# Optimization experiments

Hardware: AMD Instinct MI355X
Metric: run time of the kernel (lower is better)

Reference implementation:

```python
import jax, jax.numpy as jnp
import numpy as np

B, C, D, H = 16, 64, 512, 8
SEQ_LEN, LABEL_LEN, PRED_LEN = 1024, 512, 512
DEC_LEN = LABEL_LEN + PRED_LEN
DFF, KSIZE, FACTOR = 2048, 25, 3
E_LAYERS, D_LAYERS = 2, 1


def _pos_emb(L, d):
    pos = np.arange(L, dtype=np.float32)[:, None]
    div = np.exp(np.arange(0, d, 2, dtype=np.float32) * (-np.log(10000.0) / d))
    pe = np.zeros((L, d), np.float32)
    pe[:, 0::2] = np.sin(pos * div)
    pe[:, 1::2] = np.cos(pos * div)
    return jnp.asarray(pe)


def moving_mean(x, k=KSIZE):
    # AvgPool1d(k, stride=1) with replicate padding of (k-1)//2 at both ends
    pad = (k - 1) // 2
    xp = jnp.concatenate([jnp.repeat(x[:, :1], pad, 1), x, jnp.repeat(x[:, -1:], pad, 1)], axis=1)
    cs = jnp.cumsum(xp, axis=1)
    cs = jnp.concatenate([jnp.zeros_like(cs[:, :1]), cs], axis=1)
    return (cs[:, k:] - cs[:, :-k]) / k


def series_decomp(x):
    mm = moving_mean(x)
    return x - mm, mm


def circ_conv3(x, W):
    # Conv1d kernel=3, circular padding=1, no bias. x [B,L,Cin], W [3,Cin,Cout]
    L = x.shape[1]
    xp = jnp.concatenate([x[:, -1:], x, x[:, :1]], axis=1)
    return sum(jnp.einsum('blc,cd->bld', xp[:, k:k + L], W[k]) for k in range(3))


def my_layernorm(x, g, b):
    # LayerNorm then subtract per-sample mean over the time axis (special seasonal layernorm)
    mu = x.mean(-1, keepdims=True)
    var = x.var(-1, keepdims=True)
    xh = (x - mu) / jnp.sqrt(var + 1e-5) * g + b
    return xh - xh.mean(axis=1, keepdims=True)


def autocorrelation(q, k, v):
    # q,k,v: [B,L,H,E]. FFT cross-correlation, top-k lag selection, time-delay aggregation.
    L = q.shape[1]
    qf = jnp.fft.rfft(q.transpose(0, 2, 3, 1), axis=-1)
    kf = jnp.fft.rfft(k.transpose(0, 2, 3, 1), axis=-1)
    corr = jnp.fft.irfft(qf * jnp.conj(kf), n=L, axis=-1)  # [B,H,E,L]
    top_k = int(FACTOR * np.log(L))
    w, delay = jax.lax.top_k(corr.mean(axis=(1, 2)), top_k)  # [B,K]
    tc = jax.nn.softmax(w, axis=-1)
    vp = v.transpose(0, 2, 3, 1)  # [B,H,E,L]
    base = jnp.arange(L)
    agg = jnp.zeros_like(vp)
    for i in range(top_k):  # small fixed K (= int(factor*log L) = 20)
        idx = (base[None, :] + delay[:, i:i + 1]) % L  # circular shift == gather on doubled values
        pattern = jnp.take_along_axis(vp, idx[:, None, None, :], axis=-1)
        agg = agg + pattern * tc[:, i][:, None, None, None]
    return agg.transpose(0, 3, 1, 2)  # [B,L,H,E]


def ac_layer(q_in, kv_in, Wq, bq, Wk, bk, Wv, bv, Wo, bo):
    Bb, L, _ = q_in.shape
    S = kv_in.shape[1]
    E = D // H
    q = (q_in @ Wq + bq).reshape(Bb, L, H, E)
    k = (kv_in @ Wk + bk).reshape(Bb, S, H, E)
    v = (kv_in @ Wv + bv).reshape(Bb, S, H, E)
    out = autocorrelation(q, k, v)  # L == S by construction here
    return out.reshape(Bb, L, D) @ Wo + bo


def _forward(x_enc, x_dec, enc_emb_w, dec_emb_w, enc_Wq, enc_bq, enc_Wk, enc_bk, enc_Wv, enc_bv, enc_Wo, enc_bo, enc_ff1, enc_ff2, enc_ng, enc_nb, dsa_Wq, dsa_bq, dsa_Wk, dsa_bk, dsa_Wv, dsa_bv, dsa_Wo, dsa_bo, dca_Wq, dca_bq, dca_Wk, dca_bk, dca_Wv, dca_bv, dca_Wo, dca_bo, dec_ff1, dec_ff2, dec_trend_w, proj_w, proj_b):
    mean = jnp.repeat(x_enc.mean(axis=1, keepdims=True), PRED_LEN, axis=1)
    zeros = jnp.zeros((x_dec.shape[0], PRED_LEN, x_dec.shape[2]), x_enc.dtype)
    seasonal_init, trend_init = series_decomp(x_enc)
    trend = jnp.concatenate([trend_init[:, -LABEL_LEN:], mean], axis=1)
    seasonal_init = jnp.concatenate([seasonal_init[:, -LABEL_LEN:], zeros], axis=1)
    # encoder (DataEmbedding_wo_temp = token circular conv + sinusoidal pos, dropout=0)
    x = circ_conv3(x_enc, enc_emb_w) + _pos_emb(SEQ_LEN, D)[None]
    for l in range(E_LAYERS):
        x = x + ac_layer(x, x, enc_Wq[l], enc_bq[l], enc_Wk[l], enc_bk[l], enc_Wv[l], enc_bv[l], enc_Wo[l], enc_bo[l])
        x, _ = series_decomp(x)
        y = jax.nn.gelu(x @ enc_ff1[l], approximate=False) @ enc_ff2[l]
        x, _ = series_decomp(x + y)
    enc_out = my_layernorm(x, enc_ng, enc_nb)
    # decoder
    xd = circ_conv3(seasonal_init, dec_emb_w) + _pos_emb(DEC_LEN, D)[None]
    for l in range(D_LAYERS):
        xd = xd + ac_layer(xd, xd, dsa_Wq[l], dsa_bq[l], dsa_Wk[l], dsa_bk[l], dsa_Wv[l], dsa_bv[l], dsa_Wo[l], dsa_bo[l])
        xd, t1 = series_decomp(xd)
        xd = xd + ac_layer(xd, enc_out, dca_Wq[l], dca_bq[l], dca_Wk[l], dca_bk[l], dca_Wv[l], dca_bv[l], dca_Wo[l], dca_bo[l])
        xd, t2 = series_decomp(xd)
        y = jax.nn.gelu(xd @ dec_ff1[l], approximate=False) @ dec_ff2[l]
        xd, t3 = series_decomp(xd + y)
        trend = trend + circ_conv3(t1 + t2 + t3, dec_trend_w[l])  # trend projection conv
    seasonal = xd @ proj_w + proj_b
    out = trend + seasonal
    return out[:, -PRED_LEN:]


def setup_inputs():
    key = jax.random.key(0)
    ks = iter(jax.random.split(key, 64))
    def n(shape, s=0.02):
        return jax.random.normal(next(ks), shape, jnp.float32) * s
    inp = {}
    inp['x_enc'] = jax.random.normal(next(ks), (B, SEQ_LEN, C), jnp.float32)
    inp['x_dec'] = jax.random.normal(next(ks), (B, DEC_LEN, C), jnp.float32)
    inp['enc_emb_w'] = n((3, C, D))
    inp['dec_emb_w'] = n((3, C, D))
    for p in ['Wq', 'Wk', 'Wv', 'Wo']:
        bp = p.replace('W', 'b')
        inp['enc_' + p] = n((E_LAYERS, D, D)); inp['enc_' + bp] = jnp.zeros((E_LAYERS, D))
        inp['dsa_' + p] = n((D_LAYERS, D, D)); inp['dsa_' + bp] = jnp.zeros((D_LAYERS, D))
        inp['dca_' + p] = n((D_LAYERS, D, D)); inp['dca_' + bp] = jnp.zeros((D_LAYERS, D))
    inp['enc_ff1'] = n((E_LAYERS, D, DFF)); inp['enc_ff2'] = n((E_LAYERS, DFF, D))
    inp['enc_ng'] = jnp.ones((D,), jnp.float32); inp['enc_nb'] = jnp.zeros((D,), jnp.float32)
    inp['dec_ff1'] = n((D_LAYERS, D, DFF)); inp['dec_ff2'] = n((D_LAYERS, DFF, D))
    inp['dec_trend_w'] = n((D_LAYERS, 3, D, C))
    inp['proj_w'] = n((D, C)); inp['proj_b'] = jnp.zeros((C,), jnp.float32)
    return inp


def reference(x_enc, x_dec, enc_emb_w, dec_emb_w, enc_Wq, enc_bq, enc_Wk, enc_bk, enc_Wv, enc_bv, enc_Wo, enc_bo, enc_ff1, enc_ff2, enc_ng, enc_nb, dsa_Wq, dsa_bq, dsa_Wk, dsa_bk, dsa_Wv, dsa_bv, dsa_Wo, dsa_bo, dca_Wq, dca_bq, dca_Wk, dca_bk, dca_Wv, dca_bv, dca_Wo, dca_bo, dec_ff1, dec_ff2, dec_trend_w, proj_w, proj_b):
    return _forward(x_enc, x_dec, enc_emb_w, dec_emb_w, enc_Wq, enc_bq, enc_Wk, enc_bk, enc_Wv, enc_bv, enc_Wo, enc_bo, enc_ff1, enc_ff2, enc_ng, enc_nb, dsa_Wq, dsa_bq, dsa_Wk, dsa_bk, dsa_Wv, dsa_bv, dsa_Wo, dsa_bo, dca_Wq, dca_bq, dca_Wk, dca_bk, dca_Wv, dca_bv, dca_Wo, dca_bo, dec_ff1, dec_ff2, dec_trend_w, proj_w, proj_b)
```

## Files before the change

### kernel.cpp

```cpp
#include <hip/hip_runtime.h>
#include <math.h>

#define B_   16
#define L_   1024
#define C_   64
#define D_   512
#define DFF_ 2048
#define TOPK_ 20

typedef float f4 __attribute__((ext_vector_type(4)));
typedef float f32x4 __attribute__((ext_vector_type(4)));
typedef short bf16x8 __attribute__((ext_vector_type(8)));
typedef unsigned short u16x8 __attribute__((ext_vector_type(8)));

__device__ __forceinline__ unsigned short f2bf(float f) {
    union { float f; unsigned u; } a; a.f = f;
    unsigned r = a.u + 0x7fff + ((a.u >> 16) & 1);
    return (unsigned short)(r >> 16);
}
__device__ __forceinline__ float bf2f(unsigned short h) {
    union { unsigned u; float f; } a; a.u = ((unsigned)h) << 16;
    return a.f;
}

__device__ __forceinline__ void gld16(const void* g, void* l) {
    __builtin_amdgcn_global_load_lds(
        (const __attribute__((address_space(1))) unsigned int*)g,
        (__attribute__((address_space(3))) unsigned int*)l, 16, 0, 0);
}


__global__ __launch_bounds__(256)
void gemm_bf16(const unsigned short* __restrict__ A, const unsigned short* __restrict__ Bt,
               float* __restrict__ Cf, unsigned short* __restrict__ Cb,
               unsigned short* __restrict__ Cl,
               const float* __restrict__ bias, int M, int N, int K, int flags, int nx)
{
    __shared__ unsigned short As[128 * 32];
    __shared__ unsigned short Bs[128 * 32];
    const int tid = threadIdx.x;
    const int wave = tid >> 6, lane = tid & 63;

    int total = gridDim.x;
    int h = blockIdx.x;
    int lidx = h;
    if ((total & 7) == 0) {
        int q = total >> 3;
        lidx = (h & 7) * q + (h >> 3);
    }
    const int bm = (lidx / nx) * 128, bn = (lidx % nx) * 128;
    const int wm = (wave >> 1) << 6, wn = (wave & 1) << 6;

    const int r0 = (wave << 5) + (lane >> 2);
    const int kq = (((lane & 3) ^ ((lane >> 3) & 3)) << 3);
    const unsigned short* Ap0 = A + (size_t)(bm + r0) * K + kq;
    const unsigned short* Ap1 = Ap0 + (size_t)16 * K;
    const unsigned short* Bp0 = Bt + (size_t)(bn + r0) * K + kq;
    const unsigned short* Bp1 = Bp0 + (size_t)16 * K;
    unsigned short* Al0 = &As[(wave << 5) * 32];
    unsigned short* Al1 = &As[((wave << 5) + 16) * 32];
    unsigned short* Bl0 = &Bs[(wave << 5) * 32];
    unsigned short* Bl1 = &Bs[((wave << 5) + 16) * 32];

    const int la = lane & 15, h4 = lane >> 4;
    const int sw = (la >> 1) & 3;
    f32x4 acc[4][4] = {};

    for (int k0 = 0; k0 < K; k0 += 32) {
        gld16(Ap0 + k0, Al0);
        gld16(Ap1 + k0, Al1);
        gld16(Bp0 + k0, Bl0);
        gld16(Bp1 + k0, Bl1);
        __syncthreads();
        bf16x8 a[4], b[4];
#pragma unroll
        for (int i = 0; i < 4; ++i) {
            a[i] = *(const bf16x8*)&As[(wm + i * 16 + la) * 32 + ((h4 ^ sw) << 3)];
            b[i] = *(const bf16x8*)&Bs[(wn + i * 16 + la) * 32 + ((h4 ^ sw) << 3)];
        }
#pragma unroll
        for (int mi = 0; mi < 4; ++mi)
#pragma unroll
            for (int ni = 0; ni < 4; ++ni)
                acc[mi][ni] = __builtin_amdgcn_mfma_f32_16x16x32_bf16(a[mi], b[ni], acc[mi][ni], 0, 0, 0);
        __syncthreads();
    }

#pragma unroll
    for (int mi = 0; mi < 4; ++mi) {
#pragma unroll
        for (int r = 0; r < 4; ++r) {
            int m = bm + wm + mi * 16 + h4 * 4 + r;
#pragma unroll
            for (int ni = 0; ni < 4; ++ni) {
                int n = bn + wn + ni * 16 + la;
                float c = acc[mi][ni][r];
                if (bias) c += bias[n];
                if (flags & 2) c = 0.5f * c * (1.0f + erff(c * 0.70710678118654752f));
                size_t o = (size_t)m * N + n;
                if (Cf) { if (flags & 1) Cf[o] += c; else Cf[o] = c; }
                if (Cb) {
                    unsigned short hb = f2bf(c);
                    Cb[o] = hb;
                    if (Cl) Cl[o] = f2bf(c - bf2f(hb));
                }
            }
        }
    }
}

__global__ __launch_bounds__(256)
void gemm_split(const unsigned short* __restrict__ A, const unsigned short* __restrict__ Bt,
                unsigned short* __restrict__ o0h, unsigned short* __restrict__ o0l, const float* __restrict__ b0,
                unsigned short* __restrict__ o1h, unsigned short* __restrict__ o1l, const float* __restrict__ b1,
                unsigned short* __restrict__ o2h, unsigned short* __restrict__ o2l, const float* __restrict__ b2,
                float* __restrict__ Gz, int M, int N, int K, int nx)
{
    __shared__ unsigned short As[128 * 32];
    __shared__ unsigned short Bs[128 * 32];
    const int tid = threadIdx.x;
    const int wave = tid >> 6, lane = tid & 63;

    int total = gridDim.x;
    int h = blockIdx.x;
    if (Gz && h < 64) Gz[h * 256 + tid] = 0.f;
    int lidx = h;
    if ((total & 7) == 0) {
        int q = total >> 3;
        lidx = (h & 7) * q + (h >> 3);
    }
    const int bm = (lidx / nx) * 128, bn = (lidx % nx) * 128;
    const int wm = (wave >> 1) << 6, wn = (wave & 1) << 6;

    const int sel = bn >> 9;
    unsigned short* oh = sel == 0 ? o0h : (sel == 1 ? o1h : o2h);
    unsigned short* ol = sel == 0 ? o0l : (sel == 1 ? o1l : o2l);
    const float* bias  = sel == 0 ? b0  : (sel == 1 ? b1  : b2);
    const int nb = bn & 511;

    const int r0 = (wave << 5) + (lane >> 2);
    const int kq = (((lane & 3) ^ ((lane >> 3) & 3)) << 3);
    const unsigned short* Ap0 = A + (size_t)(bm + r0) * K + kq;
    const unsigned short* Ap1 = Ap0 + (size_t)16 * K;
    const unsigned short* Bp0 = Bt + (size_t)(bn + r0) * K + kq;
    const unsigned short* Bp1 = Bp0 + (size_t)16 * K;
    unsigned short* Al0 = &As[(wave << 5) * 32];
    unsigned short* Al1 = &As[((wave << 5) + 16) * 32];
    unsigned short* Bl0 = &Bs[(wave << 5) * 32];
    unsigned short* Bl1 = &Bs[((wave << 5) + 16) * 32];

    const int la = lane & 15, h4 = lane >> 4;
    const int sw = (la >> 1) & 3;
    f32x4 acc[4][4] = {};

    for (int k0 = 0; k0 < K; k0 += 32) {
        gld16(Ap0 + k0, Al0);
        gld16(Ap1 + k0, Al1);
        gld16(Bp0 + k0, Bl0);
        gld16(Bp1 + k0, Bl1);
        __syncthreads();
        bf16x8 a[4], b[4];
#pragma unroll
        for (int i = 0; i < 4; ++i) {
            a[i] = *(const bf16x8*)&As[(wm + i * 16 + la) * 32 + ((h4 ^ sw) << 3)];
            b[i] = *(const bf16x8*)&Bs[(wn + i * 16 + la) * 32 + ((h4 ^ sw) << 3)];
        }
#pragma unroll
        for (int mi = 0; mi < 4; ++mi)
#pragma unroll
            for (int ni = 0; ni < 4; ++ni)
                acc[mi][ni] = __builtin_amdgcn_mfma_f32_16x16x32_bf16(a[mi], b[ni], acc[mi][ni], 0, 0, 0);
        __syncthreads();
    }

#pragma unroll
    for (int mi = 0; mi < 4; ++mi) {
#pragma unroll
        for (int r = 0; r < 4; ++r) {
            int m = bm + wm + mi * 16 + h4 * 4 + r;
#pragma unroll
            for (int ni = 0; ni < 4; ++ni) {
                int n2 = nb + wn + ni * 16 + la;
                float c = acc[mi][ni][r] + bias[n2];
                size_t o = (size_t)m * 512 + n2;
                unsigned short hb = f2bf(c);
                oh[o] = hb;
                if (ol) ol[o] = f2bf(c - bf2f(hb));
            }
        }
    }
}

__global__ __launch_bounds__(256)
void tcast_kernel(const float* __restrict__ W, unsigned short* __restrict__ Wt, int R, int Cc)
{
    __shared__ float t[32][33];
    int bx = blockIdx.x * 32, by = blockIdx.y * 32;
    int tx = threadIdx.x & 31, ty = threadIdx.x >> 5;
#pragma unroll
    for (int i = 0; i < 32; i += 8)
        t[ty + i][tx] = W[(size_t)(by + ty + i) * Cc + bx + tx];
    __syncthreads();
#pragma unroll
    for (int i = 0; i < 32; i += 8)
        Wt[(size_t)(bx + ty + i) * R + by + tx] = f2bf(t[tx][ty + i]);
}

struct P16 { const float* p[16]; };
__global__ __launch_bounds__(256)
void tcast_all(P16 srcs, unsigned short* __restrict__ dst)
{
    __shared__ float t[32][33];
    const float* W = srcs.p[blockIdx.z];
    unsigned short* Wt = dst + (size_t)blockIdx.z * 262144;
    int bx = blockIdx.x * 32, by = blockIdx.y * 32;
    int tx = threadIdx.x & 31, ty = threadIdx.x >> 5;
#pragma unroll
    for (int i = 0; i < 32; i += 8)
        t[ty + i][tx] = W[(size_t)(by + ty + i) * 512 + bx + tx];
    __syncthreads();
#pragma unroll
    for (int i = 0; i < 32; i += 8)
        Wt[(size_t)(bx + ty + i) * 512 + by + tx] = f2bf(t[tx][ty + i]);
}

__global__ __launch_bounds__(256)
void emb_kernel(const float* __restrict__ A, const float* __restrict__ W,
                float* __restrict__ Xo, unsigned short* __restrict__ Xb)
{
    __shared__ float As[66][68];
    __shared__ float Ws[3][64][64];
    const int tid = threadIdx.x;
    const int bn = blockIdx.x * 64, bm = blockIdx.y * 64;
    const int base = bm & ~1023;
    for (int i = tid; i < 66 * 64; i += 256) {
        int r = i >> 6, c = i & 63;
        int l = (bm - base) + r - 1;
        if (l < 0) l += 1024; else if (l >= 1024) l -= 1024;
        As[r][c] = A[(size_t)(base + l) * 64 + c];
    }
    for (int i = tid; i < 3 * 64 * 64; i += 256) {
        int tap = i >> 12, rem = i & 4095, k = rem >> 6, c = rem & 63;
        Ws[tap][k][c] = W[((size_t)tap * 64 + k) * 512 + bn + c];
    }
    __syncthreads();
    const int tx = tid & 15, ty = tid >> 4;
    float acc[4][4] = {};
    for (int tap = 0; tap < 3; ++tap)
        for (int k = 0; k < 64; ++k) {
            f4 bv = *(const f4*)&Ws[tap][k][tx * 4];
#pragma unroll
            for (int i = 0; i < 4; ++i) {
                float a = As[ty * 4 + i + tap][k];
#pragma unroll
                for (int j = 0; j < 4; ++j)
                    acc[i][j] = fmaf(a, bv[j], acc[i][j]);
            }
        }
#pragma unroll
    for (int i = 0; i < 4; ++i) {
        int m = bm + ty * 4 + i;
        int l = m & 1023;
#pragma unroll
        for (int j = 0; j < 4; ++j) {
            int n = bn + tx * 4 + j;
            float c = acc[i][j];
            int i2 = n & ~1;
            float div = expf(-(float)i2 * 0.017988946039015984f);
            float ang = (float)l * div;
            c += (n & 1) ? cosf(ang) : sinf(ang);
            size_t o = (size_t)m * 512 + n;
            Xo[o] = c;
            Xb[o] = f2bf(c);
        }
    }
}

__global__ __launch_bounds__(256)
void tail_kernel(const float* __restrict__ TSUM, const float* __restrict__ T1,
                 const float* __restrict__ Wt, const float* __restrict__ pw,
                 float* __restrict__ PC, float* __restrict__ PP)
{
    __shared__ float Ts[18][17];
    __shared__ float T1s[16][17];
    __shared__ float Ws[3][16][64];
    __shared__ float Ps[16][64];
    const int tid = threadIdx.x;
    const int bo = blockIdx.x * 16;
    const int kc = blockIdx.y;
    const int b = bo >> 9;
    const int lbase = (bo & 511) + 512;
    const size_t rowbase = (size_t)b << 10;
    const int tc4 = (tid & 15) * 4;
    const int tr = tid >> 4;
    const int kbeg = kc * 64, kend = kbeg + 64;
    float cacc[4] = {}, pacc[4] = {};

    for (int k0 = kbeg; k0 < kend; k0 += 16) {
        for (int i = tid; i < 18 * 16; i += 256) {
            int r = i >> 4, c = i & 15;
            int l = lbase + r - 1; if (l >= 1024) l -= 1024;
            Ts[r][c] = TSUM[(rowbase + l) * 512 + k0 + c];
        }
        {
            int r = tid >> 4, c = tid & 15;
            T1s[r][c] = T1[(rowbase + lbase + r) * 512 + k0 + c];
        }
        for (int i = tid; i < 3 * 16 * 16; i += 256) {
            int tap = i / 256, rem = i & 255, k = rem >> 4, c4 = (rem & 15) * 4;
            *(f4*)&Ws[tap][k][c4] = *(const f4*)&Wt[((size_t)tap * 512 + k0 + k) * 64 + c4];
        }
        if (tid < 256) {
            int k = tid >> 4, c4 = (tid & 15) * 4;
            *(f4*)&Ps[k][c4] = *(const f4*)&pw[(size_t)(k0 + k) * 64 + c4];
        }
        __syncthreads();
        for (int tap = 0; tap < 3; ++tap)
#pragma unroll
            for (int k = 0; k < 16; ++k) {
                f4 bv = *(const f4*)&Ws[tap][k][tc4];
                float a = Ts[tr + tap][k];
#pragma unroll
                for (int j = 0; j < 4; ++j)
                    cacc[j] = fmaf(a, bv[j], cacc[j]);
            }
#pragma unroll
        for (int k = 0; k < 16; ++k) {
            f4 bv = *(const f4*)&Ps[k][tc4];
            float a = T1s[tr][k];
#pragma unroll
            for (int j = 0; j < 4; ++j)
                pacc[j] = fmaf(a, bv[j], pacc[j]);
        }
        __syncthreads();
    }
    size_t o = ((size_t)kc * 8192 + (bo + tr)) * 64 + tc4;
    *(f4*)&PC[o] = *(f4*)cacc;
    *(f4*)&PP[o] = *(f4*)pacc;
}

__global__ __launch_bounds__(256)
void tailred_kernel(const float* __restrict__ PC, const float* __restrict__ PP,
                    const float* __restrict__ MEANC, const float* __restrict__ pb,
                    float* __restrict__ OUT)
{
    int idx = blockIdx.x * blockDim.x + threadIdx.x;
    int n = idx & 63;
    int b = idx >> 15;
    const size_t S = (size_t)8192 * 64;
    float cs = PC[idx];
    float ps = PP[idx];
#pragma unroll
    for (int s = 1; s < 8; ++s) {
        cs += PC[s * S + idx];
        ps += PP[s * S + idx];
    }
    OUT[idx] = (MEANC[(b << 6) + n] + cs) + (ps + pb[n]);
}

__global__ __launch_bounds__(256)
void corr_mfma(const unsigned short* __restrict__ Qh, const unsigned short* __restrict__ Ql,
               const unsigned short* __restrict__ Kh, const unsigned short* __restrict__ Kl,
               float* __restrict__ G)
{
    __shared__ unsigned short Qhs[128 * 32], Qls[128 * 32], Khs[128 * 32], Kls[128 * 32];
    __shared__ float diagw[4][256];
    const int tid = threadIdx.x;
    const int wave = tid >> 6, lane = tid & 63;

    const int i_ = blockIdx.x;
    const int x_ = i_ & 7, j_ = i_ >> 3;
    const int b = x_ + ((j_ >> 6) << 3);
    const int tile = j_ & 63;
    const int bt = (tile >> 3) * 128, bs = (tile & 7) * 128;

    const int wm = (wave >> 1) << 6, wn = (wave & 1) << 6;
    const size_t boff = (size_t)b << 19;

    const int r0 = (wave << 5) + (lane >> 2);
    const int kq = (((lane & 3) ^ ((lane >> 3) & 3)) << 3);
    const size_t g0 = boff + (size_t)(bt + r0) * 512 + kq;
    const size_t g1 = g0 + (size_t)16 * 512;
    const size_t p0 = boff + (size_t)(bs + r0) * 512 + kq;
    const size_t p1 = p0 + (size_t)16 * 512;
    unsigned short* qh0 = &Qhs[(wave << 5) * 32]; unsigned short* qh1 = &Qhs[((wave << 5) + 16) * 32];
    unsigned short* ql0 = &Qls[(wave << 5) * 32]; unsigned short* ql1 = &Qls[((wave << 5) + 16) * 32];
    unsigned short* kh0 = &Khs[(wave << 5) * 32]; unsigned short* kh1 = &Khs[((wave << 5) + 16) * 32];
    unsigned short* kl0 = &Kls[(wave << 5) * 32]; unsigned short* kl1 = &Kls[((wave << 5) + 16) * 32];

    float* dz = &diagw[0][0];
    dz[tid] = 0.f; dz[tid + 256] = 0.f; dz[tid + 512] = 0.f; dz[tid + 768] = 0.f;

    const int la = lane & 15, h4 = lane >> 4;
    const int sw = (la >> 1) & 3;
    f32x4 acc[4][4] = {};

    for (int k0 = 0; k0 < 512; k0 += 32) {
        gld16(Qh + g0 + k0, qh0); gld16(Qh + g1 + k0, qh1);
        gld16(Ql + g0 + k0, ql0); gld16(Ql + g1 + k0, ql1);
        gld16(Kh + p0 + k0, kh0); gld16(Kh + p1 + k0, kh1);
        gld16(Kl + p0 + k0, kl0); gld16(Kl + p1 + k0, kl1);
        __syncthreads();
        bf16x8 ah[4], al[4], bh[4], bl[4];
#pragma unroll
        for (int i = 0; i < 4; ++i) {
            int ro = (wm + i * 16 + la) * 32 + ((h4 ^ sw) << 3);
            int co = (wn + i * 16 + la) * 32 + ((h4 ^ sw) << 3);
            ah[i] = *(const bf16x8*)&Qhs[ro];
            al[i] = *(const bf16x8*)&Qls[ro];
            bh[i] = *(const bf16x8*)&Khs[co];
            bl[i] = *(const bf16x8*)&Kls[co];
        }
#pragma unroll
        for (int mi = 0; mi < 4; ++mi)
#pragma unroll
            for (int ni = 0; ni < 4; ++ni) {
                acc[mi][ni] = __builtin_amdgcn_mfma_f32_16x16x32_bf16(ah[mi], bh[ni], acc[mi][ni], 0, 0, 0);
                acc[mi][ni] = __builtin_amdgcn_mfma_f32_16x16x32_bf16(ah[mi], bl[ni], acc[mi][ni], 0, 0, 0);
                acc[mi][ni] = __builtin_amdgcn_mfma_f32_16x16x32_bf16(al[mi], bh[ni], acc[mi][ni], 0, 0, 0);
            }
        __syncthreads();
    }

    float rbin[7][4] = {};
#pragma unroll
    for (int mi = 0; mi < 4; ++mi)
#pragma unroll
        for (int ni = 0; ni < 4; ++ni)
#pragma unroll
            for (int r = 0; r < 4; ++r)
                rbin[mi - ni + 3][r] += acc[mi][ni][r];

    const int base = (wm - wn) + 4 * h4 - la + 127;
#pragma unroll
    for (int d = 0; d < 7; ++d)
#pragma unroll
        for (int r = 0; r < 4; ++r)
            atomicAdd(&diagw[wave][base + 16 * (d - 3) + r], rbin[d][r]);
    __syncthreads();
    if (tid < 255) {
        float s = diagw[0][tid] + diagw[1][tid] + diagw[2][tid] + diagw[3][tid];
        int n = (bt - bs + tid - 127) & 1023;
        atomicAdd(&G[(b << 10) + n], s);
    }
}

__global__ __launch_bounds__(256)
void topk_kernel(const float* __restrict__ G, int* __restrict__ delay,
                 float* __restrict__ tc)
{
    __shared__ float vals[1024];
    __shared__ float pw[4];
    __shared__ int   pwi[4];
    __shared__ float wsel[TOPK_];
    __shared__ int   isel[TOPK_];
    const int b = blockIdx.x, tid = threadIdx.x;
    const int lane = tid & 63, wid = tid >> 6;
    for (int i = tid; i < 1024; i += 256) vals[i] = G[(b << 10) + i] * (1.0f / 512.0f);
    __syncthreads();
    for (int it = 0; it < TOPK_; ++it) {
        float bv = -INFINITY; int bi = 0;
#pragma unroll
        for (int u = 0; u < 4; ++u) {
            int i = tid * 4 + u;
            float v = vals[i];
            if (v > bv) { bv = v; bi = i; }
        }
#pragma unroll
        for (int o = 32; o > 0; o >>= 1) {
            float ov = __shfl_xor(bv, o, 64);
            int   oi = __shfl_xor(bi, o, 64);
            if (ov > bv || (ov == bv && oi < bi)) { bv = ov; bi = oi; }
        }
        if (lane == 0) { pw[wid] = bv; pwi[wid] = bi; }
        __syncthreads();
        if (tid == 0) {
            float m = pw[0]; int mi = pwi[0];
#pragma unroll
            for (int t = 1; t < 4; ++t)
                if (pw[t] > m || (pw[t] == m && pwi[t] < mi)) { m = pw[t]; mi = pwi[t]; }
            wsel[it] = m; isel[it] = mi;
            vals[mi] = -INFINITY;
        }
        __syncthreads();
    }
    if (tid == 0) {
        float m = wsel[0];
#pragma unroll
        for (int i = 1; i < TOPK_; ++i) m = fmaxf(m, wsel[i]);
        float e[TOPK_], s = 0.f;
#pragma unroll
        for (int i = 0; i < TOPK_; ++i) { e[i] = expf(wsel[i] - m); s += e[i]; }
        float inv = 1.0f / s;
#pragma unroll
        for (int i = 0; i < TOPK_; ++i) {
            tc[b * TOPK_ + i] = e[i] * inv;
            delay[b * TOPK_ + i] = isel[i];
        }
    }
}

__global__ void agg_kernel(const unsigned short* __restrict__ V, const int* __restrict__ delay,
                           const float* __restrict__ tc, unsigned short* __restrict__ out)
{
    int idx = (blockIdx.x * blockDim.x + threadIdx.x) * 8;
    int d = idx & 511;
    int l = (idx >> 9) & 1023;
    int b = idx >> 19;
    const unsigned short* Vb = V + ((size_t)b << 19);
    float s[8] = {};
#pragma unroll
    for (int i = 0; i < TOPK_; ++i) {
        int row = (l + delay[b * TOPK_ + i]) & 1023;
        float w = tc[b * TOPK_ + i];
        u16x8 v = *(const u16x8*)&Vb[((size_t)row << 9) + d];
#pragma unroll
        for (int j = 0; j < 8; ++j)
            s[j] = fmaf(w, bf2f(v[j]), s[j]);
    }
    u16x8 o;
#pragma unroll
    for (int j = 0; j < 8; ++j) o[j] = f2bf(s[j]);
    *(u16x8*)&out[idx] = o;
}

__global__ void decomp_kernel(const float* __restrict__ x, float* __restrict__ seas,
                              unsigned short* __restrict__ seasb,
                              float* __restrict__ trend, int Bn, int Ln, int Ch,
                              int nseg, int tmode)
{
    int idx = blockIdx.x * blockDim.x + threadIdx.x;
    int total = Bn * Ch * nseg;
    if (idx >= total) return;
    int ch = idx % Ch;
    int rest = idx / Ch;
    int seg = rest % nseg;
    int b = rest / nseg;
    int segL = Ln / nseg;
    int l0 = seg * segL;
    const float* xp = x + (size_t)b * Ln * Ch + ch;
    float* sp = seas + (size_t)b * Ln * Ch + ch;
    unsigned short* bp = seasb ? seasb + (size_t)b * Ln * Ch + ch : nullptr;
    float* tp = trend ? trend + (size_t)b * Ln * Ch + ch : nullptr;
    float s = 0.f;
    for (int j = -12; j <= 12; ++j) {
        int t = l0 + j;
        t = t < 0 ? 0 : (t > Ln - 1 ? Ln - 1 : t);
        s += xp[(size_t)t * Ch];
    }
    for (int l = l0; l < l0 + segL; ++l) {
        float mm = s * (1.0f / 25.0f);
        float v = xp[(size_t)l * Ch] - mm;
        sp[(size_t)l * Ch] = v;
        if (bp) bp[(size_t)l * Ch] = f2bf(v);
        if (tmode == 1) tp[(size_t)l * Ch] = mm;
        else if (tmode == 2) tp[(size_t)l * Ch] += mm;
        int ta = l + 13; if (ta > Ln - 1) ta = Ln - 1;
        int ts = l - 12; if (ts < 0) ts = 0;
        s += xp[(size_t)ta * Ch] - xp[(size_t)ts * Ch];
    }
}

__global__ __launch_bounds__(256)
void lnrow_kernel(const float* __restrict__ x, const float* __restrict__ g,
                  const float* __restrict__ bv, float* __restrict__ out)
{
    __shared__ float sh1[4], sh2[4];
    int row = blockIdx.x, tid = threadIdx.x;
    const float* xr = x + ((size_t)row << 9);
    float v0 = xr[tid], v1 = xr[tid + 256];
    float s = v0 + v1, q = v0 * v0 + v1 * v1;
#pragma unroll
    for (int o = 32; o > 0; o >>= 1) {
        s += __shfl_down(s, o, 64);
        q += __shfl_down(q, o, 64);
    }
    int wid = tid >> 6;
    if ((tid & 63) == 0) { sh1[wid] = s; sh2[wid] = q; }
    __syncthreads();
    if (tid == 0) {
        sh1[0] = sh1[0] + sh1[1] + sh1[2] + sh1[3];
        sh2[0] = sh2[0] + sh2[1] + sh2[2] + sh2[3];
    }
    __syncthreads();
    float mu = sh1[0] * (1.0f / 512.0f);
    float var = sh2[0] * (1.0f / 512.0f) - mu * mu;
    float inv = rsqrtf(var + 1e-5f);
    out[((size_t)row << 9) + tid] = (v0 - mu) * inv * g[tid] + bv[tid];
    out[((size_t)row << 9) + tid + 256] = (v1 - mu) * inv * g[tid + 256] + bv[tid + 256];
}

__global__ void colmean_kernel(const float* __restrict__ x, float* __restrict__ m)
{
    int idx = blockIdx.x * blockDim.x + threadIdx.x;
    if (idx >= B_ * D_) return;
    int b = idx >> 9, d = idx & 511;
    const float* xp = x + ((size_t)b << 19) + d;
    float s = 0.f;
    for (int l = 0; l < L_; ++l) s += xp[(size_t)l << 9];
    m[idx] = s * (1.0f / 1024.0f);
}

__global__ void colsub_kernel(const float* __restrict__ x, const float* __restrict__ m,
                              unsigned short* __restrict__ out)
{
    int idx = blockIdx.x * blockDim.x + threadIdx.x;
    int d = idx & 511;
    int b = idx >> 19;
    out[idx] = f2bf(x[idx] - m[(b << 9) + d]);
}

__global__ void meanx_kernel(const float* __restrict__ x, float* __restrict__ m)
{
    int idx = blockIdx.x * blockDim.x + threadIdx.x;
    if (idx >= B_ * C_) return;
    int b = idx >> 6, c = idx & 63;
    const float* xp = x + (size_t)b * L_ * C_ + c;
    float s = 0.f;
    for (int l = 0; l < L_; ++l) s += xp[(size_t)l << 6];
    m[idx] = s * (1.0f / 1024.0f);
}

__global__ void builddec_kernel(const float* __restrict__ seenc, float* __restrict__ seasin)
{
    int idx = blockIdx.x * blockDim.x + threadIdx.x;
    int c = idx & 63;
    int l = (idx >> 6) & 1023;
    int b = idx >> 16;
    if (l < 512) {
        int src = (b << 16) + ((512 + l) << 6) + c;
        seasin[idx] = seenc[src];
    } else {
        seasin[idx] = 0.f;
    }
}

extern "C" void kernel_launch(void* const* d_in, const int* in_sizes, int n_in,
                              void* d_out, int out_size, void* d_ws, size_t ws_size,
                              hipStream_t stream)
{
    auto F = [&](int i) { return (const float*)d_in[i]; };
    const float* x_enc     = F(0);
    const float* enc_emb_w = F(2);
    const float* dec_emb_w = F(3);
    const float* enc_Wq = F(4);  const float* enc_bq = F(5);
    const float* dsa_Wq = F(6);  const float* dsa_bq = F(7);
    const float* dca_Wq = F(8);  const float* dca_bq = F(9);
    const float* enc_Wk = F(10); const float* enc_bk = F(11);
    const float* dsa_Wk = F(12); const float* dsa_bk = F(13);
    const float* dca_Wk = F(14); const float* dca_bk = F(15);
    const float* enc_Wv = F(16); const float* enc_bv = F(17);
    const float* dsa_Wv = F(18); const float* dsa_bv = F(19);
    const float* dca_Wv = F(20); const float* dca_bv = F(21);
    const float* enc_Wo = F(22); const float* enc_bo = F(23);
    const float* dsa_Wo = F(24); const float* dsa_bo = F(25);
    const float* dca_Wo = F(26); const float* dca_bo = F(27);
    const float* enc_ff1 = F(28); const float* enc_ff2 = F(29);
    const float* enc_ng = F(30);  const float* enc_nb = F(31);
    const float* dec_ff1 = F(32); const float* dec_ff2 = F(33);
    const float* dec_trend_w = F(34);
    const float* proj_w = F(35);  const float* proj_b = F(36);

    constexpr size_t F512 = (size_t)B_ * L_ * D_;
    constexpr size_t F64  = (size_t)B_ * L_ * C_;
    constexpr size_t SMALL = 1024 + 16384 + 320 + 320 + 8192;
    constexpr size_t WTSA_N = 16 * 262144;
    constexpr size_t WTSF_N = 2 * 1024 * 1024;
    size_t need = (3 * F512 + 2 * F64 + SMALL) * 4 + (8 * F512 + WTSA_N + WTSF_N) * 2;
    if (ws_size < need) return;

    float* X      = (float*)d_ws;
    float* T1     = X + F512;
    float* TSUM   = T1 + F512;
    float* SEASIN = TSUM + F512;
    float* TREND  = SEASIN + F64;
    float* MEANC  = TREND + F64;
    float* G      = MEANC + 1024;
    float* TCW    = G + 16384;
    int*   DEL    = (int*)(TCW + 320);
    float* LNMEAN = (float*)(DEL + 320);
    unsigned short* AB   = (unsigned short*)(LNMEAN + 8192);
    unsigned short* EB   = AB + F512;
    unsigned short* VB   = EB + F512;
    unsigned short* HB   = VB + F512;
    unsigned short* QHI  = HB + F512;
    unsigned short* QLO  = QHI + F512;
    unsigned short* KHI  = QLO + F512;
    unsigned short* KLO  = KHI + F512;
    unsigned short* WTSA = KLO + F512;
    unsigned short* WTSF = WTSA + WTSA_N;
    float* OUT = (float*)d_out;

    const int M = B_ * L_;

    auto mgemm = [&](const unsigned short* A, const unsigned short* Bt, float* Cf,
                     unsigned short* Cb, unsigned short* Cl, const float* bias,
                     int Mm, int Nn, int Kk, int flags) {
        int nx = Nn / 128;
        int total = nx * (Mm / 128);
        gemm_bf16<<<total, 256, 0, stream>>>(A, Bt, Cf, Cb, Cl, bias, Mm, Nn, Kk, flags, nx);
    };
    auto tcast = [&](const float* W, unsigned short* Wt, int R, int Cc) {
        tcast_kernel<<<dim3(Cc / 32, R / 32), 256, 0, stream>>>(W, Wt, R, Cc);
    };
    auto corr_topk_agg = [&]() {
        corr_mfma<<<1024, 256, 0, stream>>>(QHI, QLO, KHI, KLO, G);
        topk_kernel<<<16, 256, 0, stream>>>(G, DEL, TCW);
        agg_kernel<<<(int)(F512 / 8 / 256), 256, 0, stream>>>(VB, DEL, TCW, HB);
    };
    auto attn_self = [&](const unsigned short* xin, int slotbase,
                         const float* bq, const float* bk, const float* bvp, const float* bo,
                         float* resid) {
        gemm_split<<<12 * 128, 256, 0, stream>>>(xin, WTSA + (size_t)slotbase * 262144,
            QHI, QLO, bq, KHI, KLO, bk, VB, nullptr, bvp, G, M, 1536, 512, 12);
        corr_topk_agg();
        mgemm(HB, WTSA + (size_t)(slotbase + 3) * 262144, resid, nullptr, nullptr, bo, M, 512, 512, 1);
    };
    auto attn_cross = [&](const unsigned short* qin, const unsigned short* kvin, int slotbase,
                          const float* bq, const float* bk, const float* bvp, const float* bo,
                          float* resid) {
        mgemm(qin, WTSA + (size_t)slotbase * 262144, nullptr, QHI, QLO, bq, M, 512, 512, 0);
        gemm_split<<<8 * 128, 256, 0, stream>>>(kvin, WTSA + (size_t)(slotbase + 1) * 262144,
            KHI, KLO, bk, VB, nullptr, bvp, nullptr, nullptr, nullptr, G, M, 1024, 512, 8);
        corr_topk_agg();
        mgemm(HB, WTSA + (size_t)(slotbase + 3) * 262144, resid, nullptr, nullptr, bo, M, 512, 512, 1);
    };
    auto ffblock = [&](const unsigned short* xin, const float* W1, const float* W2, float* resid) {
        unsigned short* Wf1 = WTSF;
        unsigned short* Wf2 = WTSF + 1048576;
        unsigned short* HFULL = QHI;
        tcast(W1, Wf1, 512, 2048);
        tcast(W2, Wf2, 2048, 512);
        mgemm(xin, Wf1, nullptr, HFULL, nullptr, nullptr, M, 2048, 512, 2);
        mgemm(HFULL, Wf2, resid, nullptr, nullptr, nullptr, M, 512, 2048, 1);
    };

    {
        P16 srcs;
        for (int l = 0; l < 2; ++l) {
            srcs.p[l * 4 + 0] = enc_Wq + (size_t)l * 262144;
            srcs.p[l * 4 + 1] = enc_Wk + (size_t)l * 262144;
            srcs.p[l * 4 + 2] = enc_Wv + (size_t)l * 262144;
            srcs.p[l * 4 + 3] = enc_Wo + (size_t)l * 262144;
        }
        srcs.p[8]  = dsa_Wq; srcs.p[9]  = dsa_Wk; srcs.p[10] = dsa_Wv; srcs.p[11] = dsa_Wo;
        srcs.p[12] = dca_Wq; srcs.p[13] = dca_Wk; srcs.p[14] = dca_Wv; srcs.p[15] = dca_Wo;
        tcast_all<<<dim3(16, 16, 16), 256, 0, stream>>>(srcs, WTSA);
    }

    float* SEENC = (float*)QHI;
    decomp_kernel<<<(B_ * C_ * 64 + 255) / 256, 256, 0, stream>>>(x_enc, SEENC, nullptr, nullptr, B_, L_, C_, 64, 0);
    meanx_kernel<<<(B_ * C_ + 255) / 256, 256, 0, stream>>>(x_enc, MEANC);
    builddec_kernel<<<(int)(F64 / 256), 256, 0, stream>>>(SEENC, SEASIN);

    emb_kernel<<<dim3(8, 256), 256, 0, stream>>>(x_enc, enc_emb_w, X, AB);

    for (int l = 0; l < 2; ++l) {
        attn_self(AB, l * 4,
                  enc_bq + l * D_, enc_bk + l * D_, enc_bv + l * D_, enc_bo + l * D_, X);
        decomp_kernel<<<(B_ * D_ * 64 + 255) / 256, 256, 0, stream>>>(X, T1, AB, nullptr, B_, L_, D_, 64, 0);
        ffblock(AB, enc_ff1 + (size_t)l * D_ * DFF_, enc_ff2 + (size_t)l * DFF_ * D_, T1);
        decomp_kernel<<<(B_ * D_ * 64 + 255) / 256, 256, 0, stream>>>(T1, X, AB, nullptr, B_, L_, D_, 64, 0);
    }
    lnrow_kernel<<<M, 256, 0, stream>>>(X, enc_ng, enc_nb, T1);
    colmean_kernel<<<(B_ * D_ + 255) / 256, 256, 0, stream>>>(T1, LNMEAN);
    colsub_kernel<<<(int)(F512 / 256), 256, 0, stream>>>(T1, LNMEAN, EB);

    float* XD = X;
    emb_kernel<<<dim3(8, 256), 256, 0, stream>>>(SEASIN, dec_emb_w, XD, AB);

    attn_self(AB, 8, dsa_bq, dsa_bk, dsa_bv, dsa_bo, XD);
    decomp_kernel<<<(B_ * D_ * 64 + 255) / 256, 256, 0, stream>>>(XD, T1, AB, TSUM, B_, L_, D_, 64, 1);

    attn_cross(AB, EB, 12, dca_bq, dca_bk, dca_bv, dca_bo, T1);
    decomp_kernel<<<(B_ * D_ * 64 + 255) / 256, 256, 0, stream>>>(T1, XD, AB, TSUM, B_, L_, D_, 64, 2);

    ffblock(AB, dec_ff1, dec_ff2, XD);
    decomp_kernel<<<(B_ * D_ * 64 + 255) / 256, 256, 0, stream>>>(XD, T1, nullptr, TSUM, B_, L_, D_, 64, 2);

    float* PART_C = (float*)QHI;
    float* PART_P = PART_C + (size_t)8 * 8192 * 64;
    tail_kernel<<<dim3(512, 8), 256, 0, stream>>>(TSUM, T1, dec_trend_w, proj_w, PART_C, PART_P);
    tailred_kernel<<<2048, 256, 0, stream>>>(PART_C, PART_P, MEANC, proj_b, OUT);
}
```

Baseline: 1.863 ms.

## Double-buffer LDS tiles in corr_mfma to overlap global loads with MFMA

The correlation GEMM kernel now keeps two LDS buffers per operand and issues the global-to-LDS loads for the next K-slice before computing on the current one. The goal is to hide global memory latency behind the MFMA work instead of stalling at a barrier every iteration. This doubles the LDS footprint to about 68 KB per block, which may reduce occupancy. Correctness depends on the barrier placement in the unchanged loop tail.

```diff
diff --git a/kernel.cpp b/kernel.cpp
--- a/kernel.cpp
+++ b/kernel.cpp
@@ -363,7 +363,7 @@
                const unsigned short* __restrict__ Kh, const unsigned short* __restrict__ Kl,
                float* __restrict__ G)
 {
-    __shared__ unsigned short Qhs[128 * 32], Qls[128 * 32], Khs[128 * 32], Kls[128 * 32];
+    __shared__ unsigned short Qhs[2 * 4096], Qls[2 * 4096], Khs[2 * 4096], Kls[2 * 4096];
     __shared__ float diagw[4][256];
     const int tid = threadIdx.x;
     const int wave = tid >> 6, lane = tid & 63;
@@ -383,10 +383,8 @@
     const size_t g1 = g0 + (size_t)16 * 512;
     const size_t p0 = boff + (size_t)(bs + r0) * 512 + kq;
     const size_t p1 = p0 + (size_t)16 * 512;
-    unsigned short* qh0 = &Qhs[(wave << 5) * 32]; unsigned short* qh1 = &Qhs[((wave << 5) + 16) * 32];
-    unsigned short* ql0 = &Qls[(wave << 5) * 32]; unsigned short* ql1 = &Qls[((wave << 5) + 16) * 32];
-    unsigned short* kh0 = &Khs[(wave << 5) * 32]; unsigned short* kh1 = &Khs[((wave << 5) + 16) * 32];
-    unsigned short* kl0 = &Kls[(wave << 5) * 32]; unsigned short* kl1 = &Kls[((wave << 5) + 16) * 32];
+    const int wb0 = (wave << 5) * 32;
+    const int wb1 = ((wave << 5) + 16) * 32;
 
     float* dz = &diagw[0][0];
     dz[tid] = 0.f; dz[tid + 256] = 0.f; dz[tid + 512] = 0.f; dz[tid + 768] = 0.f;
@@ -395,17 +393,30 @@
     const int sw = (la >> 1) & 3;
     f32x4 acc[4][4] = {};
 
-    for (int k0 = 0; k0 < 512; k0 += 32) {
-        gld16(Qh + g0 + k0, qh0); gld16(Qh + g1 + k0, qh1);
-        gld16(Ql + g0 + k0, ql0); gld16(Ql + g1 + k0, ql1);
-        gld16(Kh + p0 + k0, kh0); gld16(Kh + p1 + k0, kh1);
-        gld16(Kl + p0 + k0, kl0); gld16(Kl + p1 + k0, kl1);
-        __syncthreads();
+    {
+        const int k0 = 0;
+        gld16(Qh + g0 + k0, &Qhs[wb0]); gld16(Qh + g1 + k0, &Qhs[wb1]);
+        gld16(Ql + g0 + k0, &Qls[wb0]); gld16(Ql + g1 + k0, &Qls[wb1]);
+        gld16(Kh + p0 + k0, &Khs[wb0]); gld16(Kh + p1 + k0, &Khs[wb1]);
+        gld16(Kl + p0 + k0, &Kls[wb0]); gld16(Kl + p1 + k0, &Kls[wb1]);
+    }
+    __syncthreads();
+
+    for (int t = 0; t < 16; ++t) {
+        if (t < 15) {
+            const int k0 = (t + 1) << 5;
+            const int lo = ((t + 1) & 1) << 12;
+            gld16(Qh + g0 + k0, &Qhs[lo + wb0]); gld16(Qh + g1 + k0, &Qhs[lo + wb1]);
+            gld16(Ql + g0 + k0, &Qls[lo + wb0]); gld16(Ql + g1 + k0, &Qls[lo + wb1]);
+            gld16(Kh + p0 + k0, &Khs[lo + wb0]); gld16(Kh + p1 + k0, &Khs[lo + wb1]);
+            gld16(Kl + p0 + k0, &Kls[lo + wb0]); gld16(Kl + p1 + k0, &Kls[lo + wb1]);
+        }
+        const int cb = (t & 1) << 12;
         bf16x8 ah[4], al[4], bh[4], bl[4];
 #pragma unroll
         for (int i = 0; i < 4; ++i) {
-            int ro = (wm + i * 16 + la) * 32 + ((h4 ^ sw) << 3);
-            int co = (wn + i * 16 + la) * 32 + ((h4 ^ sw) << 3);
+            int ro = cb + (wm + i * 16 + la) * 32 + ((h4 ^ sw) << 3);
+            int co = cb + (wn + i * 16 + la) * 32 + ((h4 ^ sw) << 3);
             ah[i] = *(const bf16x8*)&Qhs[ro];
             al[i] = *(const bf16x8*)&Qls[ro];
             bh[i] = *(const bf16x8*)&Khs[co];
```

Result: no change. 1.868 ms (+0.3%).
